# Optimization experiments

Measured on AMD Instinct MI355X. Metric: run time of the kernel, lower is better.

Reference implementation:

```python
import jax, jax.numpy as jnp
import numpy as np
from jax import lax

BN_EPS = 1e-5

def _conv(x, w, groups=1, pad=0):
    return lax.conv_general_dilated(
        x, w, window_strides=(1, 1), padding=[(pad, pad), (pad, pad)],
        dimension_numbers=('NCHW', 'OIHW', 'NCHW'), feature_group_count=groups)

def _gather2d(imgf, yi, xi, H, W):
    # imgf: [B,C,H*W] flattened image; yi, xi: [B,C,H,W] int32 corner indices
    valid = (yi >= 0) & (yi < H) & (xi >= 0) & (xi < W)
    yc = jnp.clip(yi, 0, H - 1)
    xc = jnp.clip(xi, 0, W - 1)
    idx = (yc * W + xc).reshape(imgf.shape[0], imgf.shape[1], -1)
    v = jnp.take_along_axis(imgf, idx, axis=2).reshape(yi.shape)
    return jnp.where(valid, v, 0.0)

def _bilinear_sample(img, y, x):
    # img: [B,C,H,W]; y, x: [B,C,H,W] float sample coords (zero outside)
    B, C, H, W = img.shape
    imgf = img.reshape(B, C, H * W)
    y0 = jnp.floor(y)
    x0 = jnp.floor(x)
    wy = y - y0  # weight for y1 corner
    wx = x - x0
    y0i = y0.astype(jnp.int32); y1i = y0i + 1
    x0i = x0.astype(jnp.int32); x1i = x0i + 1
    v00 = _gather2d(imgf, y0i, x0i, H, W)
    v01 = _gather2d(imgf, y0i, x1i, H, W)
    v10 = _gather2d(imgf, y1i, x0i, H, W)
    v11 = _gather2d(imgf, y1i, x1i, H, W)
    return ((1 - wy) * (1 - wx) * v00 + (1 - wy) * wx * v01
            + wy * (1 - wx) * v10 + wy * wx * v11)

def setup_inputs() -> dict:
    key = jax.random.key(0)
    ks = jax.random.split(key, 6)
    B, C, OC, H, W = 4, 64, 64, 256, 256
    return {
        'x': jax.random.normal(ks[0], (B, C, H, W), jnp.float32),
        'dw_weight': jax.random.normal(ks[1], (C, 1, 3, 3), jnp.float32) * 0.2,
        'pw_weight': jax.random.normal(ks[2], (3 * C, C, 1, 1), jnp.float32) * 0.1,
        'weight': jax.random.normal(ks[3], (OC, C, 1, 1), jnp.float32) * 0.1,
        'bias': jax.random.normal(ks[4], (OC,), jnp.float32) * 0.1,
        'gamma': jnp.ones((OC,), jnp.float32),
        'beta': jnp.zeros((OC,), jnp.float32),
    }

def reference(x, dw_weight, pw_weight, weight, bias, gamma, beta):
    B, C, H, W = x.shape
    # DWConv2d: depthwise 3x3 (pad 1) then pointwise 1x1 -> 3C channels
    om = _conv(_conv(x, dw_weight, groups=C, pad=1), pw_weight)
    offset_y = om[:, :C]
    offset_x = om[:, C:2 * C]
    modulator = 2.0 * jax.nn.sigmoid(om[:, 2 * C:])
    max_off = max(H, W) // 4
    offset = jnp.clip(jnp.concatenate([offset_y, offset_x], axis=1), -max_off, max_off)
    # torchvision deform_conv2d layout: [B, og*2, H, W] interleaved (y, x) per offset group
    off = offset.reshape(B, C, 2, H, W)
    hh = jnp.arange(H, dtype=x.dtype)[:, None]
    ww = jnp.arange(W, dtype=x.dtype)[None, :]
    sy = hh + off[:, :, 0]  # [B,C,H,W]
    sx = ww + off[:, :, 1]
    sampled = _bilinear_sample(x, sy, sx) * modulator
    w2 = weight.reshape(weight.shape[0], C)  # 1x1 kernel -> [OC, C]
    out = jnp.einsum('oc,bchw->bohw', w2, sampled) + bias[None, :, None, None]
    # BatchNorm2d (training-mode batch stats) + exact GELU
    mean = out.mean(axis=(0, 2, 3), keepdims=True)
    var = out.var(axis=(0, 2, 3), keepdims=True)
    out = (out - mean) * lax.rsqrt(var + BN_EPS)
    out = out * gamma[None, :, None, None] + beta[None, :, None, None]
    return jax.nn.gelu(out, approximate=False)
```

## Files before the change

kernel.cpp:

```cpp
#include <hip/hip_runtime.h>

#define B_  4
#define C_  64
#define H_  256
#define W_  256
#define HW_ 65536
#define NPIX_ (B_*HW_)
#define NELEM_ (B_*C_*HW_)

#define OMS 200
#define TS  72

typedef __attribute__((ext_vector_type(8))) short short8;
typedef __attribute__((ext_vector_type(4))) float floatx4;
typedef __attribute__((ext_vector_type(2))) __fp16 h2f;

static __device__ __forceinline__ unsigned short f2bf(float f){
  unsigned u = __float_as_uint(f);
  u += 0x7fff + ((u >> 16) & 1);
  return (unsigned short)(u >> 16);
}
static __device__ __forceinline__ float bf2f(unsigned short s){
  return __uint_as_float(((unsigned)s) << 16);
}
static __device__ __forceinline__ unsigned pack2(float a, float b){
  return (unsigned)f2bf(a) | ((unsigned)f2bf(b) << 16);
}

__global__ __launch_bounds__(256) void k_dwconv(
    const float* __restrict__ x,
    const float* __restrict__ dwW,
    const float* __restrict__ pw,
    const float* __restrict__ w2,
    unsigned short* __restrict__ wB,
    float* __restrict__ stats0,
    unsigned short* __restrict__ xB,
    unsigned short* __restrict__ t)
{
  int tid = threadIdx.x;
  if (blockIdx.x < 64){
    int i = blockIdx.x*256 + tid;
    wB[i] = f2bf(i < 12288 ? pw[i] : w2[i - 12288]);
  } else if (blockIdx.x == 64){
#pragma unroll
    for (int k = 0; k < 16; ++k) stats0[k*256 + tid] = 0.f;
  }

  int bid = ((blockIdx.x & 7) << 9) + (blockIdx.x >> 3);
  int b    = bid >> 10;
  int tile = bid & 1023;
  int h    = tile >> 2;
  int w0   = (tile & 3) << 6;
  int p  = tid & 63;
  int cg = tid >> 6;
  int wg = w0 + p;

  int rm = (h > 0   ? h-1 : 0) << 8;
  int r0 = h << 8;
  int rp = (h < 255 ? h+1 : 255) << 8;
  float vm = (h > 0)   ? 1.f : 0.f;
  float vp = (h < 255) ? 1.f : 0.f;

  int st = min(max(wg - 1, 0), 253);
  int d  = wg - st;
  bool d0 = (d == 0), d2 = (d == 2);

  int om = (rm + st) << 2;
  int oc = (r0 + st) << 2;
  int op = (rp + st) << 2;

  const char* plane0 = (const char*)(x + ((size_t)(b*C_ + cg*16) << 16));

  unsigned pk[8];
#pragma unroll
  for (int ib = 0; ib < 4; ++ib){
    float3 v[4][3];
#pragma unroll
    for (int j = 0; j < 4; ++j){
      const char* pl = plane0 + (((size_t)(ib*4 + j)) << 18);
      __builtin_memcpy(&v[j][0], pl + om, 12);
      __builtin_memcpy(&v[j][1], pl + oc, 12);
      __builtin_memcpy(&v[j][2], pl + op, 12);
    }
    __builtin_amdgcn_sched_barrier(0);
#pragma unroll
    for (int j = 0; j < 4; ++j){
      int i = ib*4 + j;
      int c = cg*16 + i;
      const float* wp = dwW + c*9;
      float acc = 0.f, ctr = 0.f;
#pragma unroll
      for (int r = 0; r < 3; ++r){
        float3 f = v[j][r];
        float xl = d0 ? 0.f : (d2 ? f.y : f.x);
        float xc = d0 ? f.x : (d2 ? f.z : f.y);
        float xr = d2 ? 0.f : (d0 ? f.y : f.z);
        float rowscale = (r == 0) ? vm : (r == 2 ? vp : 1.f);
        acc += rowscale * (wp[r*3+0]*xl + wp[r*3+1]*xc + wp[r*3+2]*xr);
        if (r == 1) ctr = xc;
      }
      xB[((size_t)(b*C_ + c) << 16) + r0 + wg] = f2bf(ctr);
      unsigned short bv = f2bf(acc);
      if (i & 1) pk[i>>1] |= ((unsigned)bv << 16);
      else       pk[i>>1]  = (unsigned)bv;
    }
  }
  size_t rowbase = ((size_t)bid*64 + p)*64 + cg*16;
  uint4 u0; u0.x = pk[0]; u0.y = pk[1]; u0.z = pk[2]; u0.w = pk[3];
  uint4 u1; u1.x = pk[4]; u1.y = pk[5]; u1.z = pk[6]; u1.w = pk[7];
  *(uint4*)(t + rowbase)     = u0;
  *(uint4*)(t + rowbase + 8) = u1;
}

__global__ __launch_bounds__(256, 4) void k_fuse(
    const unsigned short* __restrict__ xB,
    const unsigned short* __restrict__ t,
    const unsigned short* __restrict__ pwB,
    const unsigned short* __restrict__ w2B,
    unsigned short* __restrict__ outB,
    float* __restrict__ gsumS,
    float* __restrict__ gsqS)
{
  __shared__ __align__(16) char lds[25600];
  unsigned short* OM = (unsigned short*)lds;
  unsigned short* T  = (unsigned short*)lds;
  float* red1 = (float*)(lds + 9216);
  float* red2 = (float*)(lds + 10240);

  int tid = threadIdx.x;
  int bid = ((blockIdx.x & 7) << 9) + (blockIdx.x >> 3);
  int wv = tid >> 6, lane = tid & 63;
  int mrow = lane & 15, q = lane >> 4;
  int px0 = bid*64;
  int pxw = px0 + wv*16;

  short8 bfrag[2];
#pragma unroll
  for (int kb = 0; kb < 2; ++kb)
    bfrag[kb] = *(const short8*)(t + (size_t)(pxw + mrow)*64 + kb*32 + q*8);

  floatx4 acc[12];
#pragma unroll
  for (int mt = 0; mt < 12; ++mt) acc[mt] = (floatx4){0.f,0.f,0.f,0.f};
#pragma unroll
  for (int kb = 0; kb < 2; ++kb)
#pragma unroll
    for (int mt = 0; mt < 12; ++mt){
      short8 af = *(const short8*)(pwB + (mt*16 + mrow)*64 + kb*32 + q*8);
      acc[mt] = __builtin_amdgcn_mfma_f32_16x16x32_bf16(af, bfrag[kb], acc[mt], 0, 0, 0);
    }

  {
    int omrow = (wv*16 + mrow)*OMS;
#pragma unroll
    for (int mt = 0; mt < 12; ++mt){
      uint2 u; u.x = pack2(acc[mt][0], acc[mt][1]); u.y = pack2(acc[mt][2], acc[mt][3]);
      *(uint2*)(OM + omrow + mt*16 + q*4) = u;
    }
  }
  __syncthreads();

  unsigned pk[8];
  {
    int pl = tid & 63;
    int cg = tid >> 6;
    int px = px0 + pl;
    int b = px >> 16;
    int p = px & (HW_-1);
    int h = p >> 8, w = p & (W_-1);

    const char* xbyte = (const char*)(xB + ((size_t)(b*C_ + cg*16) << 16));
    float hf = (float)h, wf = (float)w;

    const uint4* ob = (const uint4*)(OM + pl*OMS + cg*32);
    uint4 oA = ob[0], oB = ob[1], oC = ob[2], oD = ob[3];
    const uint4* mb = (const uint4*)(OM + pl*OMS + 128 + cg*16);
    uint4 mA = mb[0], mB = mb[1];
    unsigned pr[16] = {oA.x,oA.y,oA.z,oA.w, oB.x,oB.y,oB.z,oB.w,
                       oC.x,oC.y,oC.z,oC.w, oD.x,oD.y,oD.z,oD.w};
    unsigned md[8]  = {mA.x,mA.y,mA.z,mA.w, mB.x,mB.y,mB.z,mB.w};

    h2f wrv[16];
    h2f wcv[16];
    unsigned ad0[16], ad1[16];

#pragma unroll
    for (int i = 0; i < 16; ++i){
      unsigned pair = pr[i];
      float oy = __uint_as_float(pair << 16);
      float ox = __uint_as_float(pair & 0xffff0000u);
      float mm = __uint_as_float((i & 1) ? (md[i>>1] & 0xffff0000u)
                                         : (md[i>>1] << 16));
      float mod = 2.f * __builtin_amdgcn_rcpf(1.f + __expf(-mm));
      oy = fminf(fmaxf(oy, -64.f), 64.f);
      ox = fminf(fmaxf(ox, -64.f), 64.f);
      float sy = hf + oy, sx = wf + ox;
      float y0f = floorf(sy), x0f = floorf(sx);
      float wy = sy - y0f, wxr = sx - x0f;
      int y0 = (int)y0f, x0 = (int)x0f;
      int yc0 = min(max(y0,     0), 255);
      int yc1 = min(max(y0 + 1, 0), 255);
      int xc  = min(max(x0, 0), 254);
      bool y0v = ((unsigned)y0       < 256u);
      bool y1v = ((unsigned)(y0 + 1) < 256u);
      bool x0v = ((unsigned)x0       < 256u);
      bool x1v = ((unsigned)(x0 + 1) < 256u);
      bool x0lo = (x0 == xc);
      float r0 = y0v ? (1.f - wy) * mod : 0.f;
      float r1 = y1v ? wy * mod : 0.f;
      float c0w = x0v ? (1.f - wxr) : 0.f;
      float c1w = x1v ? wxr : 0.f;
      float cA = x0lo ? c0w : c1w;
      float cB = x0lo ? c1w : c0w;
      wrv[i] = __builtin_amdgcn_cvt_pkrtz(r0, r1);
      wcv[i] = __builtin_amdgcn_cvt_pkrtz(cA, cB);
      unsigned cb = ((unsigned)i) << 17;
      ad0[i] = cb + ((unsigned)yc0 << 9) + ((unsigned)xc << 1);
      ad1[i] = cb + ((unsigned)yc1 << 9) + ((unsigned)xc << 1);
    }

    unsigned pu0[16], pu1[16];
#pragma unroll
    for (int i = 0; i < 16; ++i){
      __builtin_memcpy(&pu0[i], xbyte + ad0[i], 4);
      __builtin_memcpy(&pu1[i], xbyte + ad1[i], 4);
    }
    __builtin_amdgcn_sched_barrier(0);

#pragma unroll
    for (int i = 0; i < 16; ++i){
      float lo0 = __uint_as_float(pu0[i] << 16);
      float hi0 = __uint_as_float(pu0[i] & 0xffff0000u);
      float lo1 = __uint_as_float(pu1[i] << 16);
      float hi1 = __uint_as_float(pu1[i] & 0xffff0000u);
      float cA = (float)wcv[i].x, cB = (float)wcv[i].y;
      float r0 = (float)wrv[i].x, r1 = (float)wrv[i].y;
      float s0 = cA*lo0 + cB*hi0;
      float s1 = cA*lo1 + cB*hi1;
      float sres = r0*s0 + r1*s1;
      unsigned short bv = f2bf(sres);
      if (i & 1) pk[i>>1] |= ((unsigned)bv << 16);
      else       pk[i>>1]  = (unsigned)bv;
    }
  }
  __syncthreads();

  {
    int pl = tid & 63, cg = tid >> 6;
    uint4 u0; u0.x = pk[0]; u0.y = pk[1]; u0.z = pk[2]; u0.w = pk[3];
    uint4 u1; u1.x = pk[4]; u1.y = pk[5]; u1.z = pk[6]; u1.w = pk[7];
    *(uint4*)(T + pl*TS + cg*16)     = u0;
    *(uint4*)(T + pl*TS + cg*16 + 8) = u1;
  }
  __syncthreads();

  short8 a2[2];
#pragma unroll
  for (int kb = 0; kb < 2; ++kb)
    a2[kb] = *(const short8*)(T + (wv*16 + mrow)*TS + kb*32 + q*8);

  floatx4 acc2[4];
#pragma unroll
  for (int nt = 0; nt < 4; ++nt) acc2[nt] = (floatx4){0.f,0.f,0.f,0.f};
#pragma unroll
  for (int kb = 0; kb < 2; ++kb)
#pragma unroll
    for (int nt = 0; nt < 4; ++nt){
      short8 bf = *(const short8*)(w2B + (nt*16 + mrow)*64 + kb*32 + q*8);
      acc2[nt] = __builtin_amdgcn_mfma_f32_16x16x32_bf16(a2[kb], bf, acc2[nt], 0, 0, 0);
    }

  int b   = pxw >> 16;
  int hw0 = pxw & (HW_-1);
#pragma unroll
  for (int nt = 0; nt < 4; ++nt){
    int och = nt*16 + mrow;
    float a0 = acc2[nt][0], a1 = acc2[nt][1], a2v = acc2[nt][2], a3 = acc2[nt][3];
    uint2 u; u.x = pack2(a0, a1); u.y = pack2(a2v, a3);
    *(uint2*)(outB + ((size_t)(b*C_ + och) << 16) + hw0 + q*4) = u;
    float s1 = a0 + a1 + a2v + a3;
    float s2 = a0*a0 + a1*a1 + a2v*a2v + a3*a3;
    s1 += __shfl_xor(s1, 16, 64);  s2 += __shfl_xor(s2, 16, 64);
    s1 += __shfl_xor(s1, 32, 64);  s2 += __shfl_xor(s2, 32, 64);
    if (q == 0){ red1[wv*64 + och] = s1; red2[wv*64 + och] = s2; }
  }
  __syncthreads();
  if (tid < 64){
    float t1 = red1[tid] + red1[64+tid] + red1[128+tid] + red1[192+tid];
    float t2 = red2[tid] + red2[64+tid] + red2[128+tid] + red2[192+tid];
    int slot = blockIdx.x & 31;
    atomicAdd(&gsumS[slot*64 + tid], t1);
    atomicAdd(&gsqS[slot*64 + tid], t2);
  }
}

static __device__ __forceinline__ float gelu1(float a){
  float u = a*a;
  float wv = fmaf(u*a, -0.0713548162726f, a * -1.5957691216f);
  return a * __builtin_amdgcn_rcpf(1.f + __expf(wv));
}

__global__ __launch_bounds__(256) void k_bn_gelu(
    const uint4* __restrict__ outB4,
    const float* __restrict__ gsumS,
    const float* __restrict__ gsqS,
    const float* __restrict__ gamma,
    const float* __restrict__ beta,
    float4* __restrict__ y4)
{
  int i = blockIdx.x*256 + threadIdx.x;
  int och = (i >> 13) & 63;
  float s1 = 0.f, s2 = 0.f;
#pragma unroll
  for (int s = 0; s < 32; ++s){ s1 += gsumS[s*64 + och]; s2 += gsqS[s*64 + och]; }
  float mean = s1 * (1.f/(float)NPIX_);
  float var  = s2 * (1.f/(float)NPIX_) - mean*mean;
  float sc = gamma[och] * rsqrtf(var + 1e-5f);
  float sh = beta[och] - mean*sc;

  uint4 u = outB4[i];
  float e[8];
  e[0] = bf2f((unsigned short)(u.x & 0xffffu)); e[1] = bf2f((unsigned short)(u.x >> 16));
  e[2] = bf2f((unsigned short)(u.y & 0xffffu)); e[3] = bf2f((unsigned short)(u.y >> 16));
  e[4] = bf2f((unsigned short)(u.z & 0xffffu)); e[5] = bf2f((unsigned short)(u.z >> 16));
  e[6] = bf2f((unsigned short)(u.w & 0xffffu)); e[7] = bf2f((unsigned short)(u.w >> 16));
  float4 o0, o1;
  o0.x = gelu1(fmaf(e[0], sc, sh));
  o0.y = gelu1(fmaf(e[1], sc, sh));
  o0.z = gelu1(fmaf(e[2], sc, sh));
  o0.w = gelu1(fmaf(e[3], sc, sh));
  o1.x = gelu1(fmaf(e[4], sc, sh));
  o1.y = gelu1(fmaf(e[5], sc, sh));
  o1.z = gelu1(fmaf(e[6], sc, sh));
  o1.w = gelu1(fmaf(e[7], sc, sh));
  y4[2*i]   = o0;
  y4[2*i+1] = o1;
}

extern "C" void kernel_launch(void* const* d_in, const int* in_sizes, int n_in,
                              void* d_out, int out_size, void* d_ws, size_t ws_size,
                              hipStream_t stream)
{
  (void)in_sizes; (void)n_in; (void)out_size; (void)ws_size;
  const float* x     = (const float*)d_in[0];
  const float* dw    = (const float*)d_in[1];
  const float* pw    = (const float*)d_in[2];
  const float* w2    = (const float*)d_in[3];
  const float* gamma = (const float*)d_in[5];
  const float* beta  = (const float*)d_in[6];

  char* ws = (char*)d_ws;
  unsigned short* xB    = (unsigned short*)ws;
  unsigned short* t     = (unsigned short*)(ws + 33554432);
  unsigned short* outB  = (unsigned short*)(ws + 67108864);
  float*          stats = (float*)(ws + 100663296);
  float* gsumS = stats;
  float* gsqS  = stats + 2048;
  unsigned short* wB  = (unsigned short*)(ws + 100680192);
  unsigned short* pwB = wB;
  unsigned short* w2B = wB + 12288;

  k_dwconv  <<<NPIX_/64, 256, 0, stream>>>(x, dw, pw, w2, wB, stats, xB, t);
  k_fuse    <<<NPIX_/64, 256, 0, stream>>>(xB, t, pwB, w2B, outB, gsumS, gsqS);
  k_bn_gelu <<<NELEM_/8/256, 256, 0, stream>>>((const uint4*)outB, gsumS, gsqS,
                                               gamma, beta, (float4*)d_out);
}
```

Measured before the change: 298.3 us.

## Fuse depthwise conv into main kernel and gather directly from fp32 input

Moves the depthwise 3x3 conv into the fused kernel, keeping its output in LDS rather than writing an intermediate bf16 tensor to global memory, and drops the bf16 copy of x. Bilinear gathers now read 8-byte fp32 pairs straight from the original input. This removes two large intermediate writes and re-reads in exchange for larger gather loads, more LDS per block and a tiny setup kernel. The sample loop is split into two halves of 8 channels to limit register pressure.

Measured after the change: 258.6 us. 13.3% less time.

```diff
diff --git a/kernel.cpp b/kernel.cpp
--- a/kernel.cpp
+++ b/kernel.cpp
@@ -27,25 +27,36 @@
   return (unsigned)f2bf(a) | ((unsigned)f2bf(b) << 16);
 }
 
-__global__ __launch_bounds__(256) void k_dwconv(
-    const float* __restrict__ x,
-    const float* __restrict__ dwW,
-    const float* __restrict__ pw,
-    const float* __restrict__ w2,
-    unsigned short* __restrict__ wB,
-    float* __restrict__ stats0,
-    unsigned short* __restrict__ xB,
-    unsigned short* __restrict__ t)
+__global__ __launch_bounds__(256) void k_setup(
+    const float* __restrict__ pw, const float* __restrict__ w2,
+    unsigned short* __restrict__ wB, float* __restrict__ stats0)
 {
   int tid = threadIdx.x;
   if (blockIdx.x < 64){
     int i = blockIdx.x*256 + tid;
     wB[i] = f2bf(i < 12288 ? pw[i] : w2[i - 12288]);
-  } else if (blockIdx.x == 64){
+  } else {
 #pragma unroll
     for (int k = 0; k < 16; ++k) stats0[k*256 + tid] = 0.f;
   }
-
+}
+
+__global__ __launch_bounds__(256, 4) void k_fuse(
+    const float* __restrict__ x,
+    const float* __restrict__ dwW,
+    const unsigned short* __restrict__ pwB,
+    const unsigned short* __restrict__ w2B,
+    unsigned short* __restrict__ outB,
+    float* __restrict__ gsumS,
+    float* __restrict__ gsqS)
+{
+  __shared__ __align__(16) char lds[34816];
+  unsigned short* T  = (unsigned short*)lds;
+  unsigned short* OM = (unsigned short*)(lds + 9216);
+  float* red1 = (float*)(lds + 9216);
+  float* red2 = (float*)(lds + 10240);
+
+  int tid = threadIdx.x;
   int bid = ((blockIdx.x & 7) << 9) + (blockIdx.x >> 3);
   int b    = bid >> 10;
   int tile = bid & 1023;
@@ -55,89 +66,68 @@
   int cg = tid >> 6;
   int wg = w0 + p;
 
-  int rm = (h > 0   ? h-1 : 0) << 8;
-  int r0 = h << 8;
-  int rp = (h < 255 ? h+1 : 255) << 8;
-  float vm = (h > 0)   ? 1.f : 0.f;
-  float vp = (h < 255) ? 1.f : 0.f;
-
-  int st = min(max(wg - 1, 0), 253);
-  int d  = wg - st;
-  bool d0 = (d == 0), d2 = (d == 2);
-
-  int om = (rm + st) << 2;
-  int oc = (r0 + st) << 2;
-  int op = (rp + st) << 2;
-
-  const char* plane0 = (const char*)(x + ((size_t)(b*C_ + cg*16) << 16));
-
-  unsigned pk[8];
-#pragma unroll
-  for (int ib = 0; ib < 4; ++ib){
-    float3 v[4][3];
-#pragma unroll
-    for (int j = 0; j < 4; ++j){
-      const char* pl = plane0 + (((size_t)(ib*4 + j)) << 18);
-      __builtin_memcpy(&v[j][0], pl + om, 12);
-      __builtin_memcpy(&v[j][1], pl + oc, 12);
-      __builtin_memcpy(&v[j][2], pl + op, 12);
-    }
-    __builtin_amdgcn_sched_barrier(0);
-#pragma unroll
-    for (int j = 0; j < 4; ++j){
-      int i = ib*4 + j;
-      int c = cg*16 + i;
-      const float* wp = dwW + c*9;
-      float acc = 0.f, ctr = 0.f;
-#pragma unroll
-      for (int r = 0; r < 3; ++r){
-        float3 f = v[j][r];
-        float xl = d0 ? 0.f : (d2 ? f.y : f.x);
-        float xc = d0 ? f.x : (d2 ? f.z : f.y);
-        float xr = d2 ? 0.f : (d0 ? f.y : f.z);
-        float rowscale = (r == 0) ? vm : (r == 2 ? vp : 1.f);
-        acc += rowscale * (wp[r*3+0]*xl + wp[r*3+1]*xc + wp[r*3+2]*xr);
-        if (r == 1) ctr = xc;
-      }
-      xB[((size_t)(b*C_ + c) << 16) + r0 + wg] = f2bf(ctr);
-      unsigned short bv = f2bf(acc);
-      if (i & 1) pk[i>>1] |= ((unsigned)bv << 16);
-      else       pk[i>>1]  = (unsigned)bv;
-    }
-  }
-  size_t rowbase = ((size_t)bid*64 + p)*64 + cg*16;
-  uint4 u0; u0.x = pk[0]; u0.y = pk[1]; u0.z = pk[2]; u0.w = pk[3];
-  uint4 u1; u1.x = pk[4]; u1.y = pk[5]; u1.z = pk[6]; u1.w = pk[7];
-  *(uint4*)(t + rowbase)     = u0;
-  *(uint4*)(t + rowbase + 8) = u1;
-}
-
-__global__ __launch_bounds__(256, 4) void k_fuse(
-    const unsigned short* __restrict__ xB,
-    const unsigned short* __restrict__ t,
-    const unsigned short* __restrict__ pwB,
-    const unsigned short* __restrict__ w2B,
-    unsigned short* __restrict__ outB,
-    float* __restrict__ gsumS,
-    float* __restrict__ gsqS)
-{
-  __shared__ __align__(16) char lds[25600];
-  unsigned short* OM = (unsigned short*)lds;
-  unsigned short* T  = (unsigned short*)lds;
-  float* red1 = (float*)(lds + 9216);
-  float* red2 = (float*)(lds + 10240);
-
-  int tid = threadIdx.x;
-  int bid = ((blockIdx.x & 7) << 9) + (blockIdx.x >> 3);
+  {
+    int rm = (h > 0   ? h-1 : 0) << 8;
+    int r0 = h << 8;
+    int rp = (h < 255 ? h+1 : 255) << 8;
+    float vm = (h > 0)   ? 1.f : 0.f;
+    float vp = (h < 255) ? 1.f : 0.f;
+    int st = min(max(wg - 1, 0), 253);
+    int d  = wg - st;
+    bool d0 = (d == 0), d2 = (d == 2);
+    int om = (rm + st) << 2;
+    int oc = (r0 + st) << 2;
+    int op = (rp + st) << 2;
+
+    const char* plane0 = (const char*)(x + ((size_t)(b*C_ + cg*16) << 16));
+
+    unsigned pk[8];
+#pragma unroll
+    for (int ib = 0; ib < 4; ++ib){
+      float3 v[4][3];
+#pragma unroll
+      for (int j = 0; j < 4; ++j){
+        const char* pl = plane0 + (((size_t)(ib*4 + j)) << 18);
+        __builtin_memcpy(&v[j][0], pl + om, 12);
+        __builtin_memcpy(&v[j][1], pl + oc, 12);
+        __builtin_memcpy(&v[j][2], pl + op, 12);
+      }
+      __builtin_amdgcn_sched_barrier(0);
+#pragma unroll
+      for (int j = 0; j < 4; ++j){
+        int i = ib*4 + j;
+        int c = cg*16 + i;
+        const float* wp = dwW + c*9;
+        float acc = 0.f;
+#pragma unroll
+        for (int r = 0; r < 3; ++r){
+          float3 f = v[j][r];
+          float xl = d0 ? 0.f : (d2 ? f.y : f.x);
+          float xc = d0 ? f.x : (d2 ? f.z : f.y);
+          float xr = d2 ? 0.f : (d0 ? f.y : f.z);
+          float rowscale = (r == 0) ? vm : (r == 2 ? vp : 1.f);
+          acc += rowscale * (wp[r*3+0]*xl + wp[r*3+1]*xc + wp[r*3+2]*xr);
+        }
+        unsigned short bv = f2bf(acc);
+        if (i & 1) pk[i>>1] |= ((unsigned)bv << 16);
+        else       pk[i>>1]  = (unsigned)bv;
+      }
+    }
+    uint4 u0; u0.x = pk[0]; u0.y = pk[1]; u0.z = pk[2]; u0.w = pk[3];
+    uint4 u1; u1.x = pk[4]; u1.y = pk[5]; u1.z = pk[6]; u1.w = pk[7];
+    *(uint4*)(T + p*TS + cg*16)     = u0;
+    *(uint4*)(T + p*TS + cg*16 + 8) = u1;
+  }
+  __syncthreads();
+
   int wv = tid >> 6, lane = tid & 63;
   int mrow = lane & 15, q = lane >> 4;
-  int px0 = bid*64;
-  int pxw = px0 + wv*16;
+  int pxw = bid*64 + wv*16;
 
   short8 bfrag[2];
 #pragma unroll
   for (int kb = 0; kb < 2; ++kb)
-    bfrag[kb] = *(const short8*)(t + (size_t)(pxw + mrow)*64 + kb*32 + q*8);
+    bfrag[kb] = *(const short8*)(T + (wv*16 + mrow)*TS + kb*32 + q*8);
 
   floatx4 acc[12];
 #pragma unroll
@@ -162,95 +152,83 @@
 
   unsigned pk[8];
   {
-    int pl = tid & 63;
-    int cg = tid >> 6;
-    int px = px0 + pl;
-    int b = px >> 16;
-    int p = px & (HW_-1);
-    int h = p >> 8, w = p & (W_-1);
-
-    const char* xbyte = (const char*)(xB + ((size_t)(b*C_ + cg*16) << 16));
-    float hf = (float)h, wf = (float)w;
-
-    const uint4* ob = (const uint4*)(OM + pl*OMS + cg*32);
-    uint4 oA = ob[0], oB = ob[1], oC = ob[2], oD = ob[3];
-    const uint4* mb = (const uint4*)(OM + pl*OMS + 128 + cg*16);
-    uint4 mA = mb[0], mB = mb[1];
-    unsigned pr[16] = {oA.x,oA.y,oA.z,oA.w, oB.x,oB.y,oB.z,oB.w,
-                       oC.x,oC.y,oC.z,oC.w, oD.x,oD.y,oD.z,oD.w};
-    unsigned md[8]  = {mA.x,mA.y,mA.z,mA.w, mB.x,mB.y,mB.z,mB.w};
-
-    h2f wrv[16];
-    h2f wcv[16];
-    unsigned ad0[16], ad1[16];
-
-#pragma unroll
-    for (int i = 0; i < 16; ++i){
-      unsigned pair = pr[i];
-      float oy = __uint_as_float(pair << 16);
-      float ox = __uint_as_float(pair & 0xffff0000u);
-      float mm = __uint_as_float((i & 1) ? (md[i>>1] & 0xffff0000u)
-                                         : (md[i>>1] << 16));
-      float mod = 2.f * __builtin_amdgcn_rcpf(1.f + __expf(-mm));
-      oy = fminf(fmaxf(oy, -64.f), 64.f);
-      ox = fminf(fmaxf(ox, -64.f), 64.f);
-      float sy = hf + oy, sx = wf + ox;
-      float y0f = floorf(sy), x0f = floorf(sx);
-      float wy = sy - y0f, wxr = sx - x0f;
-      int y0 = (int)y0f, x0 = (int)x0f;
-      int yc0 = min(max(y0,     0), 255);
-      int yc1 = min(max(y0 + 1, 0), 255);
-      int xc  = min(max(x0, 0), 254);
-      bool y0v = ((unsigned)y0       < 256u);
-      bool y1v = ((unsigned)(y0 + 1) < 256u);
-      bool x0v = ((unsigned)x0       < 256u);
-      bool x1v = ((unsigned)(x0 + 1) < 256u);
-      bool x0lo = (x0 == xc);
-      float r0 = y0v ? (1.f - wy) * mod : 0.f;
-      float r1 = y1v ? wy * mod : 0.f;
-      float c0w = x0v ? (1.f - wxr) : 0.f;
-      float c1w = x1v ? wxr : 0.f;
-      float cA = x0lo ? c0w : c1w;
-      float cB = x0lo ? c1w : c0w;
-      wrv[i] = __builtin_amdgcn_cvt_pkrtz(r0, r1);
-      wcv[i] = __builtin_amdgcn_cvt_pkrtz(cA, cB);
-      unsigned cb = ((unsigned)i) << 17;
-      ad0[i] = cb + ((unsigned)yc0 << 9) + ((unsigned)xc << 1);
-      ad1[i] = cb + ((unsigned)yc1 << 9) + ((unsigned)xc << 1);
-    }
-
-    unsigned pu0[16], pu1[16];
-#pragma unroll
-    for (int i = 0; i < 16; ++i){
-      __builtin_memcpy(&pu0[i], xbyte + ad0[i], 4);
-      __builtin_memcpy(&pu1[i], xbyte + ad1[i], 4);
-    }
-    __builtin_amdgcn_sched_barrier(0);
-
-#pragma unroll
-    for (int i = 0; i < 16; ++i){
-      float lo0 = __uint_as_float(pu0[i] << 16);
-      float hi0 = __uint_as_float(pu0[i] & 0xffff0000u);
-      float lo1 = __uint_as_float(pu1[i] << 16);
-      float hi1 = __uint_as_float(pu1[i] & 0xffff0000u);
-      float cA = (float)wcv[i].x, cB = (float)wcv[i].y;
-      float r0 = (float)wrv[i].x, r1 = (float)wrv[i].y;
-      float s0 = cA*lo0 + cB*hi0;
-      float s1 = cA*lo1 + cB*hi1;
-      float sres = r0*s0 + r1*s1;
-      unsigned short bv = f2bf(sres);
-      if (i & 1) pk[i>>1] |= ((unsigned)bv << 16);
-      else       pk[i>>1]  = (unsigned)bv;
+    float hf = (float)h, wf = (float)(w0 + p);
+    const char* xbyte = (const char*)(x + ((size_t)(b*C_ + cg*16) << 16));
+
+#pragma unroll
+    for (int half = 0; half < 2; ++half){
+      const uint4* ob = (const uint4*)(OM + p*OMS + cg*32 + half*16);
+      uint4 oA = ob[0], oB = ob[1];
+      uint4 mv = *(const uint4*)(OM + p*OMS + 128 + cg*16 + half*8);
+      unsigned pr[8] = {oA.x,oA.y,oA.z,oA.w, oB.x,oB.y,oB.z,oB.w};
+      unsigned md4[4] = {mv.x,mv.y,mv.z,mv.w};
+
+      h2f wrv[8], wcv[8];
+      unsigned ad0[8], ad1[8];
+
+#pragma unroll
+      for (int i = 0; i < 8; ++i){
+        unsigned pair = pr[i];
+        float oy = __uint_as_float(pair << 16);
+        float ox = __uint_as_float(pair & 0xffff0000u);
+        float mm = __uint_as_float((i & 1) ? (md4[i>>1] & 0xffff0000u)
+                                           : (md4[i>>1] << 16));
+        float mod = 2.f * __builtin_amdgcn_rcpf(1.f + __expf(-mm));
+        oy = fminf(fmaxf(oy, -64.f), 64.f);
+        ox = fminf(fmaxf(ox, -64.f), 64.f);
+        float sy = hf + oy, sx = wf + ox;
+        float y0f = floorf(sy), x0f = floorf(sx);
+        float wy = sy - y0f, wxr = sx - x0f;
+        int y0 = (int)y0f, x0 = (int)x0f;
+        int yc0 = min(max(y0,     0), 255);
+        int yc1 = min(max(y0 + 1, 0), 255);
+        int xc  = min(max(x0, 0), 254);
+        bool y0v = ((unsigned)y0       < 256u);
+        bool y1v = ((unsigned)(y0 + 1) < 256u);
+        bool x0v = ((unsigned)x0       < 256u);
+        bool x1v = ((unsigned)(x0 + 1) < 256u);
+        bool x0lo = (x0 == xc);
+        float r0 = y0v ? (1.f - wy) * mod : 0.f;
+        float r1 = y1v ? wy * mod : 0.f;
+        float c0w = x0v ? (1.f - wxr) : 0.f;
+        float c1w = x1v ? wxr : 0.f;
+        float cA = x0lo ? c0w : c1w;
+        float cB = x0lo ? c1w : c0w;
+        wrv[i] = __builtin_amdgcn_cvt_pkrtz(r0, r1);
+        wcv[i] = __builtin_amdgcn_cvt_pkrtz(cA, cB);
+        unsigned cb = ((unsigned)(half*8 + i)) << 18;
+        ad0[i] = cb + ((unsigned)yc0 << 10) + ((unsigned)xc << 2);
+        ad1[i] = cb + ((unsigned)yc1 << 10) + ((unsigned)xc << 2);
+      }
+
+      float2 pu0[8], pu1[8];
+#pragma unroll
+      for (int i = 0; i < 8; ++i){
+        __builtin_memcpy(&pu0[i], xbyte + ad0[i], 8);
+        __builtin_memcpy(&pu1[i], xbyte + ad1[i], 8);
+      }
+      __builtin_amdgcn_sched_barrier(0);
+
+#pragma unroll
+      for (int i = 0; i < 8; ++i){
+        int ci = half*8 + i;
+        float cA = (float)wcv[i].x, cB = (float)wcv[i].y;
+        float r0 = (float)wrv[i].x, r1 = (float)wrv[i].y;
+        float sres = r0*(cA*pu0[i].x + cB*pu0[i].y)
+                   + r1*(cA*pu1[i].x + cB*pu1[i].y);
+        unsigned short bv = f2bf(sres);
+        if (ci & 1) pk[ci>>1] |= ((unsigned)bv << 16);
+        else        pk[ci>>1]  = (unsigned)bv;
+      }
     }
   }
   __syncthreads();
 
   {
-    int pl = tid & 63, cg = tid >> 6;
     uint4 u0; u0.x = pk[0]; u0.y = pk[1]; u0.z = pk[2]; u0.w = pk[3];
     uint4 u1; u1.x = pk[4]; u1.y = pk[5]; u1.z = pk[6]; u1.w = pk[7];
-    *(uint4*)(T + pl*TS + cg*16)     = u0;
-    *(uint4*)(T + pl*TS + cg*16 + 8) = u1;
+    *(uint4*)(T + p*TS + cg*16)     = u0;
+    *(uint4*)(T + p*TS + cg*16 + 8) = u1;
   }
   __syncthreads();
 
@@ -270,14 +248,14 @@
       acc2[nt] = __builtin_amdgcn_mfma_f32_16x16x32_bf16(a2[kb], bf, acc2[nt], 0, 0, 0);
     }
 
-  int b   = pxw >> 16;
+  int bb  = pxw >> 16;
   int hw0 = pxw & (HW_-1);
 #pragma unroll
   for (int nt = 0; nt < 4; ++nt){
     int och = nt*16 + mrow;
     float a0 = acc2[nt][0], a1 = acc2[nt][1], a2v = acc2[nt][2], a3 = acc2[nt][3];
     uint2 u; u.x = pack2(a0, a1); u.y = pack2(a2v, a3);
-    *(uint2*)(outB + ((size_t)(b*C_ + och) << 16) + hw0 + q*4) = u;
+    *(uint2*)(outB + ((size_t)(bb*C_ + och) << 16) + hw0 + q*4) = u;
     float s1 = a0 + a1 + a2v + a3;
     float s2 = a0*a0 + a1*a1 + a2v*a2v + a3*a3;
     s1 += __shfl_xor(s1, 16, 64);  s2 += __shfl_xor(s2, 16, 64);
@@ -350,18 +328,16 @@
   const float* beta  = (const float*)d_in[6];
 
   char* ws = (char*)d_ws;
-  unsigned short* xB    = (unsigned short*)ws;
-  unsigned short* t     = (unsigned short*)(ws + 33554432);
-  unsigned short* outB  = (unsigned short*)(ws + 67108864);
-  float*          stats = (float*)(ws + 100663296);
+  unsigned short* outB  = (unsigned short*)ws;
+  float*          stats = (float*)(ws + 33554432);
   float* gsumS = stats;
   float* gsqS  = stats + 2048;
-  unsigned short* wB  = (unsigned short*)(ws + 100680192);
+  unsigned short* wB  = (unsigned short*)(ws + 33570816);
   unsigned short* pwB = wB;
   unsigned short* w2B = wB + 12288;
 
-  k_dwconv  <<<NPIX_/64, 256, 0, stream>>>(x, dw, pw, w2, wB, stats, xB, t);
-  k_fuse    <<<NPIX_/64, 256, 0, stream>>>(xB, t, pwB, w2B, outB, gsumS, gsqS);
+  k_setup   <<<65, 256, 0, stream>>>(pw, w2, wB, stats);
+  k_fuse    <<<NPIX_/64, 256, 0, stream>>>(x, dw, pwB, w2B, outB, gsumS, gsqS);
   k_bn_gelu <<<NELEM_/8/256, 256, 0, stream>>>((const uint4*)outB, gsumS, gsqS,
                                                gamma, beta, (float4*)d_out);
 }
```
